# Performance work log

Measured on AMD Instinct MI355X. Metric: run time of the kernel, lower is better.

## Reference

```python
import jax, jax.numpy as jnp
import numpy as np
from math import sqrt

LOCAL_WINDOW = 32
STRIDE = 64


def _sparse_mask(L):
    # L_Q == L_K path of DozerAttention:
    #  - local window: diagonals at offsets 0..local_window//2 (both signs)
    #  - strided: diagonals at offsets 0, stride+1, 2*(stride+1), ... (both signs)
    i = jnp.arange(L)[:, None]
    j = jnp.arange(L)[None, :]
    d = jnp.abs(i - j)
    local = d <= (LOCAL_WINDOW // 2)
    strided = (d % (STRIDE + 1)) == 0
    return (local | strided).astype(jnp.float32)  # [L, L]


def setup_inputs() -> dict:
    key = jax.random.key(0)
    B, L, H, D = 2, 2048, 8, 64
    kq, kk, kv = jax.random.split(key, 3)
    queries = jax.random.normal(kq, (B, L, H, D), dtype=jnp.float32)
    keys = jax.random.normal(kk, (B, L, H, D), dtype=jnp.float32)
    values = jax.random.normal(kv, (B, L, H, D), dtype=jnp.float32)
    # TriangularCausalMask: True above the diagonal -> masked with -inf
    causal = jnp.triu(jnp.ones((L, L), dtype=bool), k=1)
    attn_mask = jnp.broadcast_to(causal[None, None], (B, 1, L, L))
    return {"queries": queries, "keys": keys, "values": values, "attn_mask": attn_mask}


def reference(queries, keys, values, attn_mask):
    B, L, H, D = queries.shape
    scale = 1.0 / sqrt(D)
    sm = _sparse_mask(L)  # [L, L]
    # Original fills a zero-initialized dense score tensor only at selected key
    # columns per query row; equivalent to dense QK^T elementwise-masked by sm
    # (non-selected entries stay exactly 0, NOT -inf -- faithful quirk).
    scores = jnp.einsum('blhe,bshe->bhls', queries, keys) * sm  # [B,H,L,L]
    scores = jnp.where(attn_mask, -jnp.inf, scores)
    A = jax.nn.softmax(scale * scores, axis=-1)  # dropout p=0.0 in this config
    V = jnp.einsum('bhls,bshd->blhd', A, values)  # [B,L,H,D]
    return V
```

## Files before the change

kernel.cpp:

```cpp
#include <hip/hip_runtime.h>
#include <hip/hip_bf16.h>

#define B_ 2
#define L_ 2048
#define H_ 8
#define D_ 64
#define SP_ 65
#define NC_ 128
#define NH_ 16
#define RS_ 512

typedef __attribute__((ext_vector_type(8))) short bf16x8;
typedef __attribute__((ext_vector_type(16))) float f32x16;

static __device__ inline short f2bf(float x) {
    return __builtin_bit_cast(short, __float2bfloat16(x));
}

static __device__ inline bf16x8 ld8_bf16(const float* __restrict__ p) {
    float4 a = *(const float4*)p;
    float4 b = *(const float4*)(p + 4);
    bf16x8 r;
    r[0]=f2bf(a.x); r[1]=f2bf(a.y); r[2]=f2bf(a.z); r[3]=f2bf(a.w);
    r[4]=f2bf(b.x); r[5]=f2bf(b.y); r[6]=f2bf(b.z); r[7]=f2bf(b.w);
    return r;
}

static __device__ inline bf16x8 ones_frag() {
    bf16x8 r;
    short o = f2bf(1.f);
    #pragma unroll
    for (int t = 0; t < 8; ++t) r[t] = o;
    return r;
}

__global__ __launch_bounds__(256) void partials_k(const float* __restrict__ q,
                                                  const float* __restrict__ kk,
                                                  const float* __restrict__ v,
                                                  float* __restrict__ csum1,
                                                  float* __restrict__ pA,
                                                  float* __restrict__ zA,
                                                  float* __restrict__ pB,
                                                  float* __restrict__ zB,
                                                  float* __restrict__ csumH) {
    __shared__ float LDS[4608];
    int wib  = threadIdx.x >> 6;
    int lane = threadIdx.x & 63;
    int half = lane >> 5, ln = lane & 31;
    int blk  = blockIdx.x;

    if (blk < 512) {
        int tb = wib >> 1;
        int hf = wib & 1;
        int team = blk * 2 + tb;
        int bh = team >> 6;
        int T  = (team & 63) << 5;
        int h = bh & 7, b = bh >> 3;
        const size_t base = (size_t)b * L_ * RS_ + (size_t)h * D_;
        float* Pw = LDS + tb * 2176;
        int d0 = 32 * hf;

        bf16x8 bv[4];
        #pragma unroll
        for (int kb = 0; kb < 4; ++kb) {
            #pragma unroll
            for (int jj = 0; jj < 8; ++jj) {
                int jr = T - 16 + kb * 16 + half * 8 + jj;
                jr = jr < 0 ? 0 : (jr > L_ - 1 ? L_ - 1 : jr);
                bv[kb][jj] = f2bf(v[base + (size_t)jr * RS_ + d0 + ln]);
            }
        }

        const float* qrow = q + base + (size_t)(T + ln) * RS_;
        bf16x8 aq[4];
        #pragma unroll
        for (int kb = 0; kb < 4; ++kb) aq[kb] = ld8_bf16(qrow + kb * 16 + half * 8);

        int j = T - 16 + d0 + ln;
        j = j < 0 ? 0 : (j > L_ - 1 ? L_ - 1 : j);
        const float* krow = kk + base + (size_t)j * RS_;
        f32x16 acc = {};
        #pragma unroll
        for (int kb = 0; kb < 4; ++kb) {
            bf16x8 kf = ld8_bf16(krow + kb * 16 + half * 8);
            acc = __builtin_amdgcn_mfma_f32_32x32x16_bf16(aq[kb], kf, acc, 0, 0, 0);
        }

        #pragma unroll
        for (int r = 0; r < 16; ++r) {
            int m = (r & 3) + 8 * (r >> 2) + 4 * half;
            float w;
            if (hf == 0) {
                bool act = (ln >= m) && (ln <= m + 16) && (T - 16 + ln >= 0);
                w = act ? (__expf(0.125f * acc[r]) - 1.f) : 0.f;
                if ((m < 16) && (ln >= 16) && (ln <= m + 16)) w += 1.f;
            } else {
                bool act = (ln <= m - 16);
                w = act ? (__expf(0.125f * acc[r]) - 1.f) : 0.f;
                if ((m >= 16) && (ln <= m - 16)) w += 1.f;
            }
            Pw[m * 68 + d0 + ln] = w;
        }
        __syncthreads();

        f32x16 p = {}; f32x16 po = {};
        bf16x8 ones = ones_frag();
        #pragma unroll
        for (int kb = 0; kb < 4; ++kb) {
            int k0 = kb * 16 + half * 8;
            const float* pr = &Pw[ln * 68 + k0];
            float4 x = *(const float4*)pr;
            float4 y = *(const float4*)(pr + 4);
            bf16x8 ap;
            ap[0]=f2bf(x.x); ap[1]=f2bf(x.y); ap[2]=f2bf(x.z); ap[3]=f2bf(x.w);
            ap[4]=f2bf(y.x); ap[5]=f2bf(y.y); ap[6]=f2bf(y.z); ap[7]=f2bf(y.w);
            p = __builtin_amdgcn_mfma_f32_32x32x16_bf16(ap, bv[kb], p, 0, 0, 0);
            if (hf == 1)
                po = __builtin_amdgcn_mfma_f32_32x32x16_bf16(ap, ones, po, 0, 0, 0);
        }

        float* pAr = pA + (size_t)bh * L_ * D_;
        float* zAr = zA + (size_t)bh * L_;
        #pragma unroll
        for (int r = 0; r < 16; ++r) {
            int m = (r & 3) + 8 * (r >> 2) + 4 * half;
            int i = T + m;
            pAr[(size_t)i * D_ + d0 + ln] = p[r];
            if (hf == 1 && ln == 0)
                zAr[i] = po[r] - (float)((m & 15) + 1);
        }
    } else if (blk < 772) {
        int us = (blk - 512) * 4 + wib;
        int bh = us / SP_;
        int r  = us % SP_;
        int h = bh & 7, b = bh >> 3;
        const size_t base = (size_t)b * L_ * RS_ + (size_t)h * D_;
        float* Pw = LDS + wib * 1152;

        bf16x8 bv0[2], bv1[2];
        #pragma unroll
        for (int kb = 0; kb < 2; ++kb) {
            int k0 = kb * 16 + half * 8;
            #pragma unroll
            for (int jj = 0; jj < 8; ++jj) {
                int lv = r + SP_ * (k0 + jj);
                lv = lv > L_ - 1 ? L_ - 1 : lv;
                const float* vr = v + base + (size_t)lv * RS_;
                bv0[kb][jj] = f2bf(vr[ln]);
                bv1[kb][jj] = f2bf(vr[32 + ln]);
            }
        }

        int lq = r + SP_ * ln;
        int lqc = lq > L_ - 1 ? L_ - 1 : lq;
        const float* qrow = q  + base + (size_t)lqc * RS_;
        const float* krow = kk + base + (size_t)lqc * RS_;
        f32x16 acc = {};
        #pragma unroll
        for (int kb = 0; kb < 4; ++kb) {
            bf16x8 a  = ld8_bf16(qrow + kb * 16 + half * 8);
            bf16x8 bb = ld8_bf16(krow + kb * 16 + half * 8);
            acc = __builtin_amdgcn_mfma_f32_32x32x16_bf16(a, bb, acc, 0, 0, 0);
        }
        #pragma unroll
        for (int rg = 0; rg < 16; ++rg) {
            int m = (rg & 3) + 8 * (rg >> 2) + 4 * half;
            bool act = (ln < m) && (r + SP_ * m < L_);
            Pw[m * 36 + ln] = act ? (__expf(0.125f * acc[rg]) - 1.f) : 0.f;
        }
        __syncthreads();

        f32x16 p0 = {}; f32x16 p1 = {}; f32x16 po = {};
        bf16x8 ones = ones_frag();
        #pragma unroll
        for (int kb = 0; kb < 2; ++kb) {
            int k0 = kb * 16 + half * 8;
            const float* pr = &Pw[ln * 36 + k0];
            float4 x = *(const float4*)pr;
            float4 y = *(const float4*)(pr + 4);
            bf16x8 ap;
            ap[0]=f2bf(x.x); ap[1]=f2bf(x.y); ap[2]=f2bf(x.z); ap[3]=f2bf(x.w);
            ap[4]=f2bf(y.x); ap[5]=f2bf(y.y); ap[6]=f2bf(y.z); ap[7]=f2bf(y.w);
            p0 = __builtin_amdgcn_mfma_f32_32x32x16_bf16(ap, bv0[kb], p0, 0, 0, 0);
            p1 = __builtin_amdgcn_mfma_f32_32x32x16_bf16(ap, bv1[kb], p1, 0, 0, 0);
            po = __builtin_amdgcn_mfma_f32_32x32x16_bf16(ap, ones,    po, 0, 0, 0);
        }
        float* pBr = pB + (size_t)bh * L_ * D_;
        float* zBr = zB + (size_t)bh * L_;
        #pragma unroll
        for (int rg = 0; rg < 16; ++rg) {
            int m = (rg & 3) + 8 * (rg >> 2) + 4 * half;
            int l = r + SP_ * m;
            if (l < L_) {
                pBr[(size_t)l * D_ + ln]      = p0[rg];
                pBr[(size_t)l * D_ + 32 + ln] = p1[rg];
                if (ln == 0) zBr[l] = po[rg];
            }
        }
    } else if (blk < 1284) {
        int uc = (blk - 772) * 4 + wib;
        int c = uc & (NC_ - 1);
        int bh = uc >> 7;
        int h = bh & 7, b = bh >> 3;
        const float* vb = v + (size_t)(b * L_ + c * 16) * RS_ + h * D_ + lane;
        float s = 0.f;
        #pragma unroll
        for (int l = 0; l < 16; ++l) s += vb[l * RS_];
        csum1[(size_t)uc * D_ + lane] = s;
    } else {
        int uc = (blk - 1284) * 4 + wib;
        int cH = uc & (NH_ - 1);
        int bh = uc >> 4;
        int h = bh & 7, b = bh >> 3;
        const float* vb = v + (size_t)(b * L_ + cH * 128) * RS_ + h * D_ + lane;
        float s0 = 0.f, s1 = 0.f, s2 = 0.f, s3 = 0.f;
        #pragma unroll 4
        for (int l = 0; l < 128; l += 4) {
            s0 += vb[(l + 0) * RS_]; s1 += vb[(l + 1) * RS_];
            s2 += vb[(l + 2) * RS_]; s3 += vb[(l + 3) * RS_];
        }
        csumH[(size_t)uc * D_ + lane] = (s0 + s1) + (s2 + s3);
    }
}

__global__ __launch_bounds__(256) void combine_k(const float* __restrict__ csum1,
                                                 const float* __restrict__ csumH,
                                                 const float* __restrict__ pA,
                                                 const float* __restrict__ zA,
                                                 const float* __restrict__ pB,
                                                 const float* __restrict__ zB,
                                                 float* __restrict__ out) {
    int wib  = threadIdx.x >> 6;
    int lane = threadIdx.x & 63;
    int u = blockIdx.x * 4 + wib;
    int bh = u >> 8;
    int g  = u & 255;
    int i0 = g << 3;
    int c1 = i0 >> 4;
    int h = bh & 7, b = bh >> 3;

    const float* zAr = zA + (size_t)bh * L_;
    const float* zBr = zB + (size_t)bh * L_;
    float zsum[8];
    #pragma unroll
    for (int r = 0; r < 8; ++r) {
        int i = i0 + r;
        zsum[r] = zAr[i] + zBr[i] + (float)(i + 1);
    }

    int nH = c1 >> 3;
    int nR = c1 & 7;
    const float* csH = csumH + (size_t)bh * NH_ * D_ + lane;
    const float* cs1 = csum1 + ((size_t)bh * NC_ + (c1 & ~7)) * D_ + lane;
    float s0 = 0.f, s1 = 0.f, s2 = 0.f, s3 = 0.f;
    int cc = 0;
    for (; cc + 4 <= nH; cc += 4) {
        s0 += csH[(cc + 0) * D_]; s1 += csH[(cc + 1) * D_];
        s2 += csH[(cc + 2) * D_]; s3 += csH[(cc + 3) * D_];
    }
    for (; cc < nH; ++cc) s0 += csH[cc * D_];
    for (int t = 0; t < nR; ++t) {
        if (t & 1) s1 += cs1[t * D_]; else s2 += cs1[t * D_];
    }
    float pr = (s0 + s1) + (s2 + s3);

    const float* pAr = pA + (size_t)bh * L_ * D_;
    const float* pBr = pB + (size_t)bh * L_ * D_;
    const size_t obase = (size_t)b * L_ * RS_ + (size_t)h * D_;

    #pragma unroll
    for (int r = 0; r < 8; ++r) {
        int i = i0 + r;
        float num = pAr[(size_t)i * D_ + lane] + pBr[(size_t)i * D_ + lane] + pr;
        out[obase + (size_t)i * RS_ + lane] = num / zsum[r];
    }
}

extern "C" void kernel_launch(void* const* d_in, const int* in_sizes, int n_in,
                              void* d_out, int out_size, void* d_ws, size_t ws_size,
                              hipStream_t stream) {
    const float* q = (const float*)d_in[0];
    const float* k = (const float*)d_in[1];
    const float* v = (const float*)d_in[2];
    float* out = (float*)d_out;

    float* csum1 = (float*)d_ws;
    float* pA    = csum1 + (size_t)B_ * H_ * NC_ * D_;
    float* zA    = pA    + (size_t)B_ * H_ * L_ * D_;
    float* pB    = zA    + (size_t)B_ * H_ * L_;
    float* zB    = pB    + (size_t)B_ * H_ * L_ * D_;
    float* csumH = zB    + (size_t)B_ * H_ * L_;

    partials_k<<<1348, 256, 0, stream>>>(q, k, v, csum1, pA, zA, pB, zB, csumH);
    combine_k<<<1024, 256, 0, stream>>>(csum1, csumH, pA, zA, pB, zB, out);
}
```

Measured before the change: 108.9 us.

## Fuse local-window partials into combine kernel and merge column-sum passes

Moves the local-window QK/softmax/PV work out of the first kernel into the second, which now also does the final combine. The intermediate pA/zA buffers and their global round-trip are removed. The first kernel keeps the strided partials and computes the 16-row and 128-row V column sums in one pass instead of two. Block indices are swizzled across groups of 8, and the fused kernel gains extra LDS use and a second barrier. The smaller first launch may leave the GPU underused.

```diff
diff --git a/kernel.cpp b/kernel.cpp
--- a/kernel.cpp
+++ b/kernel.cpp
@@ -34,103 +34,21 @@
     return r;
 }
 
-__global__ __launch_bounds__(256) void partials_k(const float* __restrict__ q,
-                                                  const float* __restrict__ kk,
-                                                  const float* __restrict__ v,
-                                                  float* __restrict__ csum1,
-                                                  float* __restrict__ pA,
-                                                  float* __restrict__ zA,
-                                                  float* __restrict__ pB,
-                                                  float* __restrict__ zB,
-                                                  float* __restrict__ csumH) {
+__global__ __launch_bounds__(256) void pre_k(const float* __restrict__ q,
+                                             const float* __restrict__ kk,
+                                             const float* __restrict__ v,
+                                             float* __restrict__ csum1,
+                                             float* __restrict__ csumH,
+                                             float* __restrict__ pB,
+                                             float* __restrict__ zB) {
     __shared__ float LDS[4608];
     int wib  = threadIdx.x >> 6;
     int lane = threadIdx.x & 63;
     int half = lane >> 5, ln = lane & 31;
     int blk  = blockIdx.x;
 
-    if (blk < 512) {
-        int tb = wib >> 1;
-        int hf = wib & 1;
-        int team = blk * 2 + tb;
-        int bh = team >> 6;
-        int T  = (team & 63) << 5;
-        int h = bh & 7, b = bh >> 3;
-        const size_t base = (size_t)b * L_ * RS_ + (size_t)h * D_;
-        float* Pw = LDS + tb * 2176;
-        int d0 = 32 * hf;
-
-        bf16x8 bv[4];
-        #pragma unroll
-        for (int kb = 0; kb < 4; ++kb) {
-            #pragma unroll
-            for (int jj = 0; jj < 8; ++jj) {
-                int jr = T - 16 + kb * 16 + half * 8 + jj;
-                jr = jr < 0 ? 0 : (jr > L_ - 1 ? L_ - 1 : jr);
-                bv[kb][jj] = f2bf(v[base + (size_t)jr * RS_ + d0 + ln]);
-            }
-        }
-
-        const float* qrow = q + base + (size_t)(T + ln) * RS_;
-        bf16x8 aq[4];
-        #pragma unroll
-        for (int kb = 0; kb < 4; ++kb) aq[kb] = ld8_bf16(qrow + kb * 16 + half * 8);
-
-        int j = T - 16 + d0 + ln;
-        j = j < 0 ? 0 : (j > L_ - 1 ? L_ - 1 : j);
-        const float* krow = kk + base + (size_t)j * RS_;
-        f32x16 acc = {};
-        #pragma unroll
-        for (int kb = 0; kb < 4; ++kb) {
-            bf16x8 kf = ld8_bf16(krow + kb * 16 + half * 8);
-            acc = __builtin_amdgcn_mfma_f32_32x32x16_bf16(aq[kb], kf, acc, 0, 0, 0);
-        }
-
-        #pragma unroll
-        for (int r = 0; r < 16; ++r) {
-            int m = (r & 3) + 8 * (r >> 2) + 4 * half;
-            float w;
-            if (hf == 0) {
-                bool act = (ln >= m) && (ln <= m + 16) && (T - 16 + ln >= 0);
-                w = act ? (__expf(0.125f * acc[r]) - 1.f) : 0.f;
-                if ((m < 16) && (ln >= 16) && (ln <= m + 16)) w += 1.f;
-            } else {
-                bool act = (ln <= m - 16);
-                w = act ? (__expf(0.125f * acc[r]) - 1.f) : 0.f;
-                if ((m >= 16) && (ln <= m - 16)) w += 1.f;
-            }
-            Pw[m * 68 + d0 + ln] = w;
-        }
-        __syncthreads();
-
-        f32x16 p = {}; f32x16 po = {};
-        bf16x8 ones = ones_frag();
-        #pragma unroll
-        for (int kb = 0; kb < 4; ++kb) {
-            int k0 = kb * 16 + half * 8;
-            const float* pr = &Pw[ln * 68 + k0];
-            float4 x = *(const float4*)pr;
-            float4 y = *(const float4*)(pr + 4);
-            bf16x8 ap;
-            ap[0]=f2bf(x.x); ap[1]=f2bf(x.y); ap[2]=f2bf(x.z); ap[3]=f2bf(x.w);
-            ap[4]=f2bf(y.x); ap[5]=f2bf(y.y); ap[6]=f2bf(y.z); ap[7]=f2bf(y.w);
-            p = __builtin_amdgcn_mfma_f32_32x32x16_bf16(ap, bv[kb], p, 0, 0, 0);
-            if (hf == 1)
-                po = __builtin_amdgcn_mfma_f32_32x32x16_bf16(ap, ones, po, 0, 0, 0);
-        }
-
-        float* pAr = pA + (size_t)bh * L_ * D_;
-        float* zAr = zA + (size_t)bh * L_;
-        #pragma unroll
-        for (int r = 0; r < 16; ++r) {
-            int m = (r & 3) + 8 * (r >> 2) + 4 * half;
-            int i = T + m;
-            pAr[(size_t)i * D_ + d0 + ln] = p[r];
-            if (hf == 1 && ln == 0)
-                zAr[i] = po[r] - (float)((m & 15) + 1);
-        }
-    } else if (blk < 772) {
-        int us = (blk - 512) * 4 + wib;
+    if (blk < 260) {
+        int us = blk * 4 + wib;
         int bh = us / SP_;
         int r  = us % SP_;
         int h = bh & 7, b = bh >> 3;
@@ -197,82 +115,165 @@
                 if (ln == 0) zBr[l] = po[rg];
             }
         }
-    } else if (blk < 1284) {
-        int uc = (blk - 772) * 4 + wib;
-        int c = uc & (NC_ - 1);
-        int bh = uc >> 7;
-        int h = bh & 7, b = bh >> 3;
-        const float* vb = v + (size_t)(b * L_ + c * 16) * RS_ + h * D_ + lane;
-        float s = 0.f;
-        #pragma unroll
-        for (int l = 0; l < 16; ++l) s += vb[l * RS_];
-        csum1[(size_t)uc * D_ + lane] = s;
     } else {
-        int uc = (blk - 1284) * 4 + wib;
+        int uc = (blk - 260) * 4 + wib;
         int cH = uc & (NH_ - 1);
         int bh = uc >> 4;
         int h = bh & 7, b = bh >> 3;
         const float* vb = v + (size_t)(b * L_ + cH * 128) * RS_ + h * D_ + lane;
-        float s0 = 0.f, s1 = 0.f, s2 = 0.f, s3 = 0.f;
-        #pragma unroll 4
-        for (int l = 0; l < 128; l += 4) {
-            s0 += vb[(l + 0) * RS_]; s1 += vb[(l + 1) * RS_];
-            s2 += vb[(l + 2) * RS_]; s3 += vb[(l + 3) * RS_];
-        }
-        csumH[(size_t)uc * D_ + lane] = (s0 + s1) + (s2 + s3);
-    }
-}
-
-__global__ __launch_bounds__(256) void combine_k(const float* __restrict__ csum1,
-                                                 const float* __restrict__ csumH,
-                                                 const float* __restrict__ pA,
-                                                 const float* __restrict__ zA,
-                                                 const float* __restrict__ pB,
-                                                 const float* __restrict__ zB,
-                                                 float* __restrict__ out) {
+        float* c1p = csum1 + ((size_t)bh * NC_ + cH * 8) * D_ + lane;
+        float hs = 0.f;
+        #pragma unroll
+        for (int c = 0; c < 8; ++c) {
+            float s0 = 0.f, s1 = 0.f, s2 = 0.f, s3 = 0.f;
+            #pragma unroll
+            for (int l = 0; l < 16; l += 4) {
+                s0 += vb[(c * 16 + l + 0) * RS_]; s1 += vb[(c * 16 + l + 1) * RS_];
+                s2 += vb[(c * 16 + l + 2) * RS_]; s3 += vb[(c * 16 + l + 3) * RS_];
+            }
+            float s = (s0 + s1) + (s2 + s3);
+            c1p[c * D_] = s;
+            hs += s;
+        }
+        csumH[((size_t)bh * NH_ + cH) * D_ + lane] = hs;
+    }
+}
+
+__global__ __launch_bounds__(256) void local_k(const float* __restrict__ q,
+                                               const float* __restrict__ kk,
+                                               const float* __restrict__ v,
+                                               const float* __restrict__ csum1,
+                                               const float* __restrict__ csumH,
+                                               const float* __restrict__ pB,
+                                               const float* __restrict__ zB,
+                                               float* __restrict__ out) {
+    __shared__ float LDS[4672];
     int wib  = threadIdx.x >> 6;
     int lane = threadIdx.x & 63;
-    int u = blockIdx.x * 4 + wib;
-    int bh = u >> 8;
-    int g  = u & 255;
-    int i0 = g << 3;
-    int c1 = i0 >> 4;
+    int half = lane >> 5, ln = lane & 31;
+    int wid = (blockIdx.x & 7) * 64 + (blockIdx.x >> 3);
+
+    int tb = wib >> 1;
+    int hf = wib & 1;
+    int team = wid * 2 + tb;
+    int bh = team >> 6;
+    int T  = (team & 63) << 5;
     int h = bh & 7, b = bh >> 3;
-
-    const float* zAr = zA + (size_t)bh * L_;
+    const size_t base = (size_t)b * L_ * RS_ + (size_t)h * D_;
+    float* Pw = LDS + tb * 2176;
+    float* PF = LDS + 4352 + tb * 128;
+    float* ZW = LDS + 4608 + tb * 32;
+    int d0 = 32 * hf;
+
+    bf16x8 bv[4];
+    #pragma unroll
+    for (int kb = 0; kb < 4; ++kb) {
+        #pragma unroll
+        for (int jj = 0; jj < 8; ++jj) {
+            int jr = T - 16 + kb * 16 + half * 8 + jj;
+            jr = jr < 0 ? 0 : (jr > L_ - 1 ? L_ - 1 : jr);
+            bv[kb][jj] = f2bf(v[base + (size_t)jr * RS_ + d0 + ln]);
+        }
+    }
+
+    const float* qrow = q + base + (size_t)(T + ln) * RS_;
+    bf16x8 aq[4];
+    #pragma unroll
+    for (int kb = 0; kb < 4; ++kb) aq[kb] = ld8_bf16(qrow + kb * 16 + half * 8);
+
+    int j = T - 16 + d0 + ln;
+    j = j < 0 ? 0 : (j > L_ - 1 ? L_ - 1 : j);
+    const float* krow = kk + base + (size_t)j * RS_;
+    f32x16 acc = {};
+    #pragma unroll
+    for (int kb = 0; kb < 4; ++kb) {
+        bf16x8 kf = ld8_bf16(krow + kb * 16 + half * 8);
+        acc = __builtin_amdgcn_mfma_f32_32x32x16_bf16(aq[kb], kf, acc, 0, 0, 0);
+    }
+
+    #pragma unroll
+    for (int r = 0; r < 16; ++r) {
+        int m = (r & 3) + 8 * (r >> 2) + 4 * half;
+        float w;
+        if (hf == 0) {
+            bool act = (ln >= m) && (ln <= m + 16) && (T - 16 + ln >= 0);
+            w = act ? (__expf(0.125f * acc[r]) - 1.f) : 0.f;
+            if ((m < 16) && (ln >= 16) && (ln <= m + 16)) w += 1.f;
+        } else {
+            bool act = (ln <= m - 16);
+            w = act ? (__expf(0.125f * acc[r]) - 1.f) : 0.f;
+            if ((m >= 16) && (ln <= m - 16)) w += 1.f;
+        }
+        Pw[m * 68 + d0 + ln] = w;
+    }
+
+    if (hf == 0) {
+        int c1 = T >> 4;
+        int nH = c1 >> 3, nR = c1 & 7;
+        const float* csH = csumH + (size_t)bh * NH_ * D_ + lane;
+        const float* cs1 = csum1 + ((size_t)bh * NC_ + (c1 & ~7)) * D_ + lane;
+        float s0 = 0.f, s1 = 0.f, s2 = 0.f, s3 = 0.f;
+        int cc = 0;
+        for (; cc + 4 <= nH; cc += 4) {
+            s0 += csH[(cc + 0) * D_]; s1 += csH[(cc + 1) * D_];
+            s2 += csH[(cc + 2) * D_]; s3 += csH[(cc + 3) * D_];
+        }
+        for (; cc < nH; ++cc) s0 += csH[cc * D_];
+        for (int t = 0; t < nR; ++t) {
+            if (t & 1) s1 += cs1[t * D_]; else s2 += cs1[t * D_];
+        }
+        float P0 = (s0 + s1) + (s2 + s3);
+        float P1 = P0 + csum1[((size_t)bh * NC_ + c1) * D_ + lane];
+        PF[lane]      = P0;
+        PF[64 + lane] = P1;
+    }
+    __syncthreads();
+
+    const float* pBr = pB + (size_t)bh * L_ * D_;
     const float* zBr = zB + (size_t)bh * L_;
-    float zsum[8];
-    #pragma unroll
-    for (int r = 0; r < 8; ++r) {
-        int i = i0 + r;
-        zsum[r] = zAr[i] + zBr[i] + (float)(i + 1);
-    }
-
-    int nH = c1 >> 3;
-    int nR = c1 & 7;
-    const float* csH = csumH + (size_t)bh * NH_ * D_ + lane;
-    const float* cs1 = csum1 + ((size_t)bh * NC_ + (c1 & ~7)) * D_ + lane;
-    float s0 = 0.f, s1 = 0.f, s2 = 0.f, s3 = 0.f;
-    int cc = 0;
-    for (; cc + 4 <= nH; cc += 4) {
-        s0 += csH[(cc + 0) * D_]; s1 += csH[(cc + 1) * D_];
-        s2 += csH[(cc + 2) * D_]; s3 += csH[(cc + 3) * D_];
-    }
-    for (; cc < nH; ++cc) s0 += csH[cc * D_];
-    for (int t = 0; t < nR; ++t) {
-        if (t & 1) s1 += cs1[t * D_]; else s2 += cs1[t * D_];
-    }
-    float pr = (s0 + s1) + (s2 + s3);
-
-    const float* pAr = pA + (size_t)bh * L_ * D_;
-    const float* pBr = pB + (size_t)bh * L_ * D_;
-    const size_t obase = (size_t)b * L_ * RS_ + (size_t)h * D_;
-
-    #pragma unroll
-    for (int r = 0; r < 8; ++r) {
-        int i = i0 + r;
-        float num = pAr[(size_t)i * D_ + lane] + pBr[(size_t)i * D_ + lane] + pr;
-        out[obase + (size_t)i * RS_ + lane] = num / zsum[r];
+    float pbv[16], zbv[16];
+    #pragma unroll
+    for (int r = 0; r < 16; ++r) {
+        int m = (r & 3) + 8 * (r >> 2) + 4 * half;
+        int i = T + m;
+        pbv[r] = pBr[(size_t)i * D_ + d0 + ln];
+        zbv[r] = zBr[i];
+    }
+
+    f32x16 p = {}; f32x16 po = {};
+    bf16x8 ones = ones_frag();
+    #pragma unroll
+    for (int kb = 0; kb < 4; ++kb) {
+        int k0 = kb * 16 + half * 8;
+        const float* pr = &Pw[ln * 68 + k0];
+        float4 x = *(const float4*)pr;
+        float4 y = *(const float4*)(pr + 4);
+        bf16x8 ap;
+        ap[0]=f2bf(x.x); ap[1]=f2bf(x.y); ap[2]=f2bf(x.z); ap[3]=f2bf(x.w);
+        ap[4]=f2bf(y.x); ap[5]=f2bf(y.y); ap[6]=f2bf(y.z); ap[7]=f2bf(y.w);
+        p = __builtin_amdgcn_mfma_f32_32x32x16_bf16(ap, bv[kb], p, 0, 0, 0);
+        if (hf == 1)
+            po = __builtin_amdgcn_mfma_f32_32x32x16_bf16(ap, ones, po, 0, 0, 0);
+    }
+
+    if (hf == 1) {
+        #pragma unroll
+        for (int r = 0; r < 16; ++r) {
+            int m = (r & 3) + 8 * (r >> 2) + 4 * half;
+            if (ln == 0) ZW[m] = po[r] - (float)((m & 15) + 1);
+        }
+    }
+    __syncthreads();
+
+    float Pf0 = PF[d0 + ln];
+    float Pf1 = PF[64 + d0 + ln];
+    #pragma unroll
+    for (int r = 0; r < 16; ++r) {
+        int m = (r & 3) + 8 * (r >> 2) + 4 * half;
+        int i = T + m;
+        float z   = ZW[m] + zbv[r] + (float)(i + 1);
+        float num = p[r] + pbv[r] + (m < 16 ? Pf0 : Pf1);
+        out[base + (size_t)i * RS_ + d0 + ln] = num / z;
     }
 }
 
@@ -285,12 +286,10 @@
     float* out = (float*)d_out;
 
     float* csum1 = (float*)d_ws;
-    float* pA    = csum1 + (size_t)B_ * H_ * NC_ * D_;
-    float* zA    = pA    + (size_t)B_ * H_ * L_ * D_;
-    float* pB    = zA    + (size_t)B_ * H_ * L_;
+    float* pB    = csum1 + (size_t)B_ * H_ * NC_ * D_;
     float* zB    = pB    + (size_t)B_ * H_ * L_ * D_;
     float* csumH = zB    + (size_t)B_ * H_ * L_;
 
-    partials_k<<<1348, 256, 0, stream>>>(q, k, v, csum1, pA, zA, pB, zB, csumH);
-    combine_k<<<1024, 256, 0, stream>>>(csum1, csumH, pA, zA, pB, zB, out);
-}
+    pre_k<<<324, 256, 0, stream>>>(q, k, v, csum1, csumH, pB, zB);
+    local_k<<<512, 256, 0, stream>>>(q, k, v, csum1, csumH, pB, zB, out);
+}
```

New measurement: 108.9 us (median of 2 runs). About the same (-0.0%).
